# Kernel optimization log

Measured on AMD Instinct MI355X. Metric: run time of the kernel, lower is better.

The kernel has to match this reference:

```python
import jax, jax.numpy as jnp
import numpy as np

DIM = 1024
H = 16
HD = DIM // H  # 64
BASE = 10000.0


def _rope_tables(seq_len, d):
    # freqs over half-dim, then TILED (repeat) along last axis as in the torch code
    freqs = 1.0 / (BASE ** (jnp.arange(0, d, 2, dtype=jnp.float32) / d))  # [d/2]
    t = jnp.arange(seq_len, dtype=jnp.float32)
    f = jnp.outer(t, freqs)  # [S, d/2]
    cos = jnp.concatenate([jnp.cos(f), jnp.cos(f)], axis=-1)  # [S, d] (tiled, NOT interleaved)
    sin = jnp.concatenate([jnp.sin(f), jnp.sin(f)], axis=-1)
    return cos, sin


def _apply_rope(x):
    # x: [B, H, S, d]; rotation pairs adjacent elements (2i, 2i+1)
    S, d = x.shape[-2], x.shape[-1]
    cos, sin = _rope_tables(S, d)  # [S, d]
    xh = x.reshape(*x.shape[:-1], d // 2, 2)
    x_rot = jnp.stack([-xh[..., 1], xh[..., 0]], axis=-1).reshape(x.shape)
    return x * cos + x_rot * sin


def setup_inputs() -> dict:
    key = jax.random.key(0)
    ks = jax.random.split(key, 7)
    B, Sq, Sk = 16, 512, 512
    s = 0.02
    return {
        "x": jax.random.normal(ks[0], (B, Sq, DIM), jnp.float32),
        "context": jax.random.normal(ks[1], (B, Sk, DIM), jnp.float32),
        "Wq": jax.random.normal(ks[2], (DIM, DIM), jnp.float32) * s,
        "Wk": jax.random.normal(ks[3], (DIM, DIM), jnp.float32) * s,
        "Wv": jax.random.normal(ks[4], (DIM, DIM), jnp.float32) * s,
        "Wo": jax.random.normal(ks[5], (DIM, DIM), jnp.float32) * s,
        "bo": jax.random.normal(ks[6], (DIM,), jnp.float32) * s,
    }


def reference(x, context, Wq, Wk, Wv, Wo, bo):
    B, Sq, _ = x.shape
    Sk = context.shape[1]
    scale = HD ** -0.5
    # projections, split heads: [B, H, S, HD]
    q = (x @ Wq).reshape(B, Sq, H, HD).transpose(0, 2, 1, 3)
    k = (context @ Wk).reshape(B, Sk, H, HD).transpose(0, 2, 1, 3)
    v = (context @ Wv).reshape(B, Sk, H, HD).transpose(0, 2, 1, 3)
    q = _apply_rope(q)
    k = _apply_rope(k)
    attn = jax.nn.softmax(jnp.einsum("bhqd,bhkd->bhqk", q, k) * scale, axis=-1)
    out = jnp.einsum("bhqk,bhkd->bhqd", attn, v)
    out = out.transpose(0, 2, 1, 3).reshape(B, Sq, DIM)
    return out @ Wo + bo  # dropout is identity (p=0 / eval)
```

## Files before the change

kernel.cpp:

```cpp
#include <hip/hip_runtime.h>

#define DIM   1024
#define NH    16
#define HD    64
#define BATCH 16
#define SEQ   512
#define MROWS (BATCH*SEQ)
#define SL2E  0.18033688011112042f

typedef __bf16 bf16x8 __attribute__((ext_vector_type(8)));
typedef float  floatx4 __attribute__((ext_vector_type(4)));

static __device__ __forceinline__ unsigned short f2bf(float f) {
    union { float f; unsigned u; } v; v.f = f;
    unsigned u = v.u;
    return (unsigned short)((u + 0x7fffu + ((u >> 16) & 1u)) >> 16);
}

static __device__ __forceinline__ void glds16(const void* g, void* l) {
    __builtin_amdgcn_global_load_lds(
        (const __attribute__((address_space(1))) unsigned int*)g,
        (__attribute__((address_space(3))) unsigned int*)l, 16, 0, 0);
}

__global__ __launch_bounds__(256)
void rope_tab(float* __restrict__ ct, float* __restrict__ st)
{
    int id = blockIdx.x * blockDim.x + threadIdx.x;
    int d = id & (HD - 1), s = id >> 6;
    const float C = -0.41524101186092f;
    float f = exp2f((float)(d & 31) * C);
    float a = (float)s * f;
    ct[id] = cosf(a);
    st[id] = sinf(a);
}

__global__ __launch_bounds__(256)
void cvt_bf16(const float* __restrict__ X, const float* __restrict__ Cx,
              unsigned short* __restrict__ Xb, unsigned short* __restrict__ Cb)
{
    int id = blockIdx.x * blockDim.x + threadIdx.x;
    const float* src; unsigned short* dst; int e;
    if (id < (MROWS * DIM / 8)) { src = X;  dst = Xb; e = id * 8; }
    else                        { src = Cx; dst = Cb; e = (id - MROWS * DIM / 8) * 8; }
    float4 f0 = *(const float4*)&src[e];
    float4 f1 = *(const float4*)&src[e + 4];
    unsigned short o[8] = { f2bf(f0.x), f2bf(f0.y), f2bf(f0.z), f2bf(f0.w),
                            f2bf(f1.x), f2bf(f1.y), f2bf(f1.z), f2bf(f1.w) };
    *(uint4*)&dst[e] = *(const uint4*)o;
}

__global__ void transpose_w(const float* __restrict__ W0, const float* __restrict__ W1,
                            const float* __restrict__ W2, const float* __restrict__ W3,
                            unsigned short* __restrict__ T0, unsigned short* __restrict__ T1,
                            unsigned short* __restrict__ T2, unsigned short* __restrict__ T3)
{
    __shared__ float tile[32][33];
    const float* W; unsigned short* T;
    switch (blockIdx.z) {
        case 0:  W = W0; T = T0; break;
        case 1:  W = W1; T = T1; break;
        case 2:  W = W2; T = T2; break;
        default: W = W3; T = T3; break;
    }
    int n0 = blockIdx.x * 32, k0 = blockIdx.y * 32;
    int tx = threadIdx.x, ty = threadIdx.y;
    tile[ty][tx] = W[(size_t)(k0 + ty) * DIM + n0 + tx];
    __syncthreads();
    T[(size_t)(n0 + ty) * DIM + k0 + tx] = f2bf(tile[tx][ty]);
}

template <int MODE>
__global__ __launch_bounds__(256)
void gemm128(const unsigned short* __restrict__ A, const unsigned short* __restrict__ Bt,
             void* __restrict__ Out, const float* __restrict__ bias,
             const float* __restrict__ costab, const float* __restrict__ sintab)
{
    __shared__ unsigned short As[128 * 64];
    __shared__ unsigned short Bs[128 * 64];

    const int n0 = blockIdx.x * 128;
    const int m0 = blockIdx.y * 128;
    const int t  = threadIdx.x;
    const int w = t >> 6, l = t & 63;
    const int wm = w >> 1, wn = w & 1;
    const int lane16 = l & 15, quad = l >> 4;
    const int lr = l >> 3;
    const int lc = (l & 7) * 8;

    floatx4 acc[4][4];
    #pragma unroll
    for (int mi = 0; mi < 4; mi++)
        #pragma unroll
        for (int ni = 0; ni < 4; ni++) acc[mi][ni] = (floatx4){0.f, 0.f, 0.f, 0.f};

    for (int kt = 0; kt < DIM; kt += 64) {
        #pragma unroll
        for (int j = 0; j < 4; j++) {
            int ch = w * 4 + j;
            int row = ch * 8 + lr;
            glds16(A  + (size_t)(m0 + row) * DIM + kt + lc, &As[ch * 512]);
            glds16(Bt + (size_t)(n0 + row) * DIM + kt + lc, &Bs[ch * 512]);
        }
        __syncthreads();

        #pragma unroll
        for (int kk = 0; kk < 2; kk++) {
            bf16x8 af[4], bfr[4];
            #pragma unroll
            for (int mi = 0; mi < 4; mi++)
                af[mi] = *(const bf16x8*)&As[(wm * 64 + mi * 16 + lane16) * 64 + kk * 32 + quad * 8];
            #pragma unroll
            for (int ni = 0; ni < 4; ni++)
                bfr[ni] = *(const bf16x8*)&Bs[(wn * 64 + ni * 16 + lane16) * 64 + kk * 32 + quad * 8];
            #pragma unroll
            for (int mi = 0; mi < 4; mi++)
                #pragma unroll
                for (int ni = 0; ni < 4; ni++)
                    acc[mi][ni] = __builtin_amdgcn_mfma_f32_16x16x32_bf16(af[mi], bfr[ni], acc[mi][ni], 0, 0, 0);
        }
        __syncthreads();
    }

    if (MODE == 0) {
        unsigned short* O = (unsigned short*)Out;
        #pragma unroll
        for (int ni = 0; ni < 4; ni++) {
            int n = n0 + wn * 64 + ni * 16 + lane16;
            int h = n >> 6, d = n & 63;
            #pragma unroll
            for (int mi = 0; mi < 4; mi++) {
                #pragma unroll
                for (int i = 0; i < 4; i++) {
                    int m = m0 + wm * 64 + mi * 16 + quad * 4 + i;
                    int s = m & 511, b = m >> 9;
                    float v = acc[mi][ni][i];
                    float p = __shfl_xor(v, 1, 64);
                    float cs = costab[s * HD + d];
                    float sn = sintab[s * HD + d];
                    float r = (n & 1) ? fmaf(p, sn, v * cs) : fmaf(-p, sn, v * cs);
                    O[((size_t)(b * NH + h) * SEQ + s) * HD + d] = f2bf(r);
                }
            }
        }
    } else if (MODE == 1) {
        unsigned short* O = (unsigned short*)Out;
        #pragma unroll
        for (int mi = 0; mi < 4; mi++) {
            #pragma unroll
            for (int i = 0; i < 4; i++) {
                int m = m0 + wm * 64 + mi * 16 + quad * 4 + i;
                #pragma unroll
                for (int ni = 0; ni < 4; ni++) {
                    int n = n0 + wn * 64 + ni * 16 + lane16;
                    O[((size_t)(n >> 9) * DIM + m) * SEQ + (n & 511)] = f2bf(acc[mi][ni][i]);
                }
            }
        }
    } else {
        float* O = (float*)Out;
        #pragma unroll
        for (int ni = 0; ni < 4; ni++) {
            int n = n0 + wn * 64 + ni * 16 + lane16;
            float bv = bias[n];
            #pragma unroll
            for (int mi = 0; mi < 4; mi++) {
                #pragma unroll
                for (int i = 0; i < 4; i++) {
                    int m = m0 + wm * 64 + mi * 16 + quad * 4 + i;
                    O[(size_t)m * DIM + n] = acc[mi][ni][i] + bv;
                }
            }
        }
    }
}

__global__ __launch_bounds__(256)
void attn_v2(const unsigned short* __restrict__ Q, const unsigned short* __restrict__ K,
             const unsigned short* __restrict__ Vt, unsigned short* __restrict__ Out)
{
    __shared__ unsigned short Qs[64][72];
    __shared__ unsigned short Ks[64][72];
    __shared__ unsigned short Vts[64][72];
    __shared__ unsigned short Ps[64][72];

    const int id = blockIdx.x;
    const int qi = (id >> 3) & 7;
    const int bh = (id & 7) | ((id >> 6) << 3);
    const int q0 = qi * 64;
    const int t  = threadIdx.x;
    const int w = t >> 6, l = t & 63;
    const int lane16 = l & 15, quad = l >> 4;
    const size_t base = (size_t)bh * SEQ * HD;

    const int r = t >> 3, dd = (t & 7) * 8;
    *(uint4*)&Qs[r][dd]      = *(const uint4*)&Q[base + (size_t)(q0 + r) * HD + dd];
    *(uint4*)&Qs[r + 32][dd] = *(const uint4*)&Q[base + (size_t)(q0 + r + 32) * HD + dd];

    floatx4 acc_o[4];
    float lsum[4];
    #pragma unroll
    for (int c = 0; c < 4; c++) acc_o[c] = (floatx4){0.f, 0.f, 0.f, 0.f};
    #pragma unroll
    for (int i = 0; i < 4; i++) lsum[i] = 0.f;

    for (int kt = 0; kt < SEQ; kt += 64) {
        *(uint4*)&Ks[r][dd]       = *(const uint4*)&K[base + (size_t)(kt + r) * HD + dd];
        *(uint4*)&Ks[r + 32][dd]  = *(const uint4*)&K[base + (size_t)(kt + r + 32) * HD + dd];
        *(uint4*)&Vts[r][dd]      = *(const uint4*)&Vt[base + (size_t)r * SEQ + kt + dd];
        *(uint4*)&Vts[r + 32][dd] = *(const uint4*)&Vt[base + (size_t)(r + 32) * SEQ + kt + dd];
        __syncthreads();

        floatx4 sacc[4];
        #pragma unroll
        for (int c = 0; c < 4; c++) sacc[c] = (floatx4){0.f, 0.f, 0.f, 0.f};
        #pragma unroll
        for (int kk = 0; kk < 2; kk++) {
            bf16x8 a = *(const bf16x8*)&Qs[w * 16 + lane16][kk * 32 + quad * 8];
            #pragma unroll
            for (int c = 0; c < 4; c++) {
                bf16x8 b = *(const bf16x8*)&Ks[c * 16 + lane16][kk * 32 + quad * 8];
                sacc[c] = __builtin_amdgcn_mfma_f32_16x16x32_bf16(a, b, sacc[c], 0, 0, 0);
            }
        }

        #pragma unroll
        for (int i = 0; i < 4; i++) {
            #pragma unroll
            for (int c = 0; c < 4; c++) {
                float pv = exp2f(sacc[c][i] * SL2E);
                lsum[i] += pv;
                Ps[w * 16 + quad * 4 + i][c * 16 + lane16] = f2bf(pv);
            }
        }

        #pragma unroll
        for (int kk = 0; kk < 2; kk++) {
            bf16x8 a = *(const bf16x8*)&Ps[w * 16 + lane16][kk * 32 + quad * 8];
            #pragma unroll
            for (int c = 0; c < 4; c++) {
                bf16x8 b = *(const bf16x8*)&Vts[c * 16 + lane16][kk * 32 + quad * 8];
                acc_o[c] = __builtin_amdgcn_mfma_f32_16x16x32_bf16(a, b, acc_o[c], 0, 0, 0);
            }
        }
        __syncthreads();
    }

    const int b = bh >> 4, h = bh & 15;
    #pragma unroll
    for (int i = 0; i < 4; i++) {
        float rs = lsum[i];
        rs += __shfl_xor(rs, 1, 64);
        rs += __shfl_xor(rs, 2, 64);
        rs += __shfl_xor(rs, 4, 64);
        rs += __shfl_xor(rs, 8, 64);
        float inv = 1.0f / rs;
        int s = q0 + w * 16 + quad * 4 + i;
        #pragma unroll
        for (int c = 0; c < 4; c++) {
            int d = c * 16 + lane16;
            Out[((size_t)(b * SEQ + s)) * DIM + h * HD + d] = f2bf(acc_o[c][i] * inv);
        }
    }
}

extern "C" void kernel_launch(void* const* d_in, const int* in_sizes, int n_in,
                              void* d_out, int out_size, void* d_ws, size_t ws_size,
                              hipStream_t stream)
{
    const float* x   = (const float*)d_in[0];
    const float* ctx = (const float*)d_in[1];
    const float* Wq  = (const float*)d_in[2];
    const float* Wk  = (const float*)d_in[3];
    const float* Wv  = (const float*)d_in[4];
    const float* Wo  = (const float*)d_in[5];
    const float* bo  = (const float*)d_in[6];

    const size_t NW = (size_t)DIM * DIM;
    const size_t NB = (size_t)MROWS * DIM;

    unsigned short* x_bf   = (unsigned short*)d_ws;
    unsigned short* ctx_bf = x_bf + NB;
    unsigned short* WqT    = ctx_bf + NB;
    unsigned short* WkT    = WqT + NW;
    unsigned short* WvT    = WkT + NW;
    unsigned short* WoT    = WvT + NW;
    unsigned short* Kb     = WoT + NW;
    unsigned short* Vtb    = Kb + NB;
    float*          costab = (float*)(Vtb + NB);
    float*          sintab = costab + SEQ * HD;
    unsigned short* Qb     = ctx_bf;
    unsigned short* Ab     = x_bf;

    rope_tab<<<SEQ * HD / 256, 256, 0, stream>>>(costab, sintab);
    cvt_bf16<<<2 * MROWS * DIM / 8 / 256, 256, 0, stream>>>(x, ctx, x_bf, ctx_bf);
    transpose_w<<<dim3(32, 32, 4), dim3(32, 32, 1), 0, stream>>>(
        Wq, Wk, Wv, Wo, WqT, WkT, WvT, WoT);

    gemm128<0><<<dim3(DIM / 128, MROWS / 128), 256, 0, stream>>>(ctx_bf, WkT, Kb, nullptr, costab, sintab);
    gemm128<1><<<dim3(MROWS / 128, DIM / 128), 256, 0, stream>>>(WvT, ctx_bf, Vtb, nullptr, nullptr, nullptr);
    gemm128<0><<<dim3(DIM / 128, MROWS / 128), 256, 0, stream>>>(x_bf, WqT, Qb, nullptr, costab, sintab);

    attn_v2<<<2048, 256, 0, stream>>>(Qb, Kb, Vtb, Ab);

    gemm128<2><<<dim3(DIM / 128, MROWS / 128), 256, 0, stream>>>(Ab, WoT, d_out, bo, nullptr, nullptr);
}
```

Baseline: 292.4 us.

## Keep softmax probabilities in registers and double query tile per attention block

The attention kernel now computes S transposed (K as the A operand), so each lane's exp'd scores already sit in the layout the 16x16x16 bf16 MFMA expects for P. P is fed straight from registers to the PV product, which drops the Ps shared-memory round trip. Each block also handles 128 query rows instead of 64, halving the grid so every K/V tile load is reused twice, at the cost of more registers and a larger Q tile in LDS. The RoPE cos/sin tables are interleaved into a single float2 table so each GEMM epilogue element does one load instead of two.

```diff
diff --git a/kernel.cpp b/kernel.cpp
--- a/kernel.cpp
+++ b/kernel.cpp
@@ -10,6 +10,7 @@
 
 typedef __bf16 bf16x8 __attribute__((ext_vector_type(8)));
 typedef float  floatx4 __attribute__((ext_vector_type(4)));
+typedef short  short4v __attribute__((ext_vector_type(4)));
 
 static __device__ __forceinline__ unsigned short f2bf(float f) {
     union { float f; unsigned u; } v; v.f = f;
@@ -24,15 +25,14 @@
 }
 
 __global__ __launch_bounds__(256)
-void rope_tab(float* __restrict__ ct, float* __restrict__ st)
+void rope_tab(float2* __restrict__ cs)
 {
     int id = blockIdx.x * blockDim.x + threadIdx.x;
     int d = id & (HD - 1), s = id >> 6;
     const float C = -0.41524101186092f;
     float f = exp2f((float)(d & 31) * C);
     float a = (float)s * f;
-    ct[id] = cosf(a);
-    st[id] = sinf(a);
+    cs[id] = make_float2(cosf(a), sinf(a));
 }
 
 __global__ __launch_bounds__(256)
@@ -74,7 +74,7 @@
 __global__ __launch_bounds__(256)
 void gemm128(const unsigned short* __restrict__ A, const unsigned short* __restrict__ Bt,
              void* __restrict__ Out, const float* __restrict__ bias,
-             const float* __restrict__ costab, const float* __restrict__ sintab)
+             const float2* __restrict__ cstab)
 {
     __shared__ unsigned short As[128 * 64];
     __shared__ unsigned short Bs[128 * 64];
@@ -136,9 +136,8 @@
                     int s = m & 511, b = m >> 9;
                     float v = acc[mi][ni][i];
                     float p = __shfl_xor(v, 1, 64);
-                    float cs = costab[s * HD + d];
-                    float sn = sintab[s * HD + d];
-                    float r = (n & 1) ? fmaf(p, sn, v * cs) : fmaf(-p, sn, v * cs);
+                    float2 cs = cstab[s * HD + d];
+                    float r = (n & 1) ? fmaf(p, cs.y, v * cs.x) : fmaf(-p, cs.y, v * cs.x);
                     O[((size_t)(b * NH + h) * SEQ + s) * HD + d] = f2bf(r);
                 }
             }
@@ -175,91 +174,99 @@
     }
 }
 
-__global__ __launch_bounds__(256)
-void attn_v2(const unsigned short* __restrict__ Q, const unsigned short* __restrict__ K,
+__global__ __launch_bounds__(256, 4)
+void attn_v3(const unsigned short* __restrict__ Q, const unsigned short* __restrict__ K,
              const unsigned short* __restrict__ Vt, unsigned short* __restrict__ Out)
 {
-    __shared__ unsigned short Qs[64][72];
+    __shared__ unsigned short Qs[128][72];
     __shared__ unsigned short Ks[64][72];
     __shared__ unsigned short Vts[64][72];
-    __shared__ unsigned short Ps[64][72];
 
     const int id = blockIdx.x;
-    const int qi = (id >> 3) & 7;
-    const int bh = (id & 7) | ((id >> 6) << 3);
-    const int q0 = qi * 64;
+    const int qi = (id >> 3) & 3;
+    const int bh = (id & 7) | ((id >> 5) << 3);
+    const int q0 = qi * 128;
     const int t  = threadIdx.x;
     const int w = t >> 6, l = t & 63;
     const int lane16 = l & 15, quad = l >> 4;
     const size_t base = (size_t)bh * SEQ * HD;
 
-    const int r = t >> 3, dd = (t & 7) * 8;
-    *(uint4*)&Qs[r][dd]      = *(const uint4*)&Q[base + (size_t)(q0 + r) * HD + dd];
-    *(uint4*)&Qs[r + 32][dd] = *(const uint4*)&Q[base + (size_t)(q0 + r + 32) * HD + dd];
-
-    floatx4 acc_o[4];
-    float lsum[4];
+    const int sr = t >> 3, sc = (t & 7) * 8;
     #pragma unroll
-    for (int c = 0; c < 4; c++) acc_o[c] = (floatx4){0.f, 0.f, 0.f, 0.f};
+    for (int j = 0; j < 4; j++)
+        *(uint4*)&Qs[j * 32 + sr][sc] =
+            *(const uint4*)&Q[base + (size_t)(q0 + j * 32 + sr) * HD + sc];
+
+    floatx4 acc_o[2][4];
+    float lsum[2] = {0.f, 0.f};
     #pragma unroll
-    for (int i = 0; i < 4; i++) lsum[i] = 0.f;
+    for (int st = 0; st < 2; st++)
+        #pragma unroll
+        for (int dt = 0; dt < 4; dt++) acc_o[st][dt] = (floatx4){0.f, 0.f, 0.f, 0.f};
 
     for (int kt = 0; kt < SEQ; kt += 64) {
-        *(uint4*)&Ks[r][dd]       = *(const uint4*)&K[base + (size_t)(kt + r) * HD + dd];
-        *(uint4*)&Ks[r + 32][dd]  = *(const uint4*)&K[base + (size_t)(kt + r + 32) * HD + dd];
-        *(uint4*)&Vts[r][dd]      = *(const uint4*)&Vt[base + (size_t)r * SEQ + kt + dd];
-        *(uint4*)&Vts[r + 32][dd] = *(const uint4*)&Vt[base + (size_t)(r + 32) * SEQ + kt + dd];
         __syncthreads();
-
-        floatx4 sacc[4];
-        #pragma unroll
-        for (int c = 0; c < 4; c++) sacc[c] = (floatx4){0.f, 0.f, 0.f, 0.f};
-        #pragma unroll
-        for (int kk = 0; kk < 2; kk++) {
-            bf16x8 a = *(const bf16x8*)&Qs[w * 16 + lane16][kk * 32 + quad * 8];
+        *(uint4*)&Ks[sr][sc]       = *(const uint4*)&K[base + (size_t)(kt + sr) * HD + sc];
+        *(uint4*)&Ks[sr + 32][sc]  = *(const uint4*)&K[base + (size_t)(kt + sr + 32) * HD + sc];
+        *(uint4*)&Vts[sr][sc]      = *(const uint4*)&Vt[base + (size_t)sr * SEQ + kt + sc];
+        *(uint4*)&Vts[sr + 32][sc] = *(const uint4*)&Vt[base + (size_t)(sr + 32) * SEQ + kt + sc];
+        __syncthreads();
+
+        short4v pa[2][4];
+        #pragma unroll
+        for (int st = 0; st < 2; st++) {
+            floatx4 sacc[4];
+            #pragma unroll
+            for (int c = 0; c < 4; c++) sacc[c] = (floatx4){0.f, 0.f, 0.f, 0.f};
+            #pragma unroll
+            for (int kk = 0; kk < 2; kk++) {
+                bf16x8 qf = *(const bf16x8*)&Qs[st * 64 + w * 16 + lane16][kk * 32 + quad * 8];
+                #pragma unroll
+                for (int c = 0; c < 4; c++) {
+                    bf16x8 kf = *(const bf16x8*)&Ks[c * 16 + lane16][kk * 32 + quad * 8];
+                    sacc[c] = __builtin_amdgcn_mfma_f32_16x16x32_bf16(kf, qf, sacc[c], 0, 0, 0);
+                }
+            }
             #pragma unroll
             for (int c = 0; c < 4; c++) {
-                bf16x8 b = *(const bf16x8*)&Ks[c * 16 + lane16][kk * 32 + quad * 8];
-                sacc[c] = __builtin_amdgcn_mfma_f32_16x16x32_bf16(a, b, sacc[c], 0, 0, 0);
-            }
-        }
-
-        #pragma unroll
-        for (int i = 0; i < 4; i++) {
-            #pragma unroll
-            for (int c = 0; c < 4; c++) {
-                float pv = exp2f(sacc[c][i] * SL2E);
-                lsum[i] += pv;
-                Ps[w * 16 + quad * 4 + i][c * 16 + lane16] = f2bf(pv);
-            }
-        }
-
-        #pragma unroll
-        for (int kk = 0; kk < 2; kk++) {
-            bf16x8 a = *(const bf16x8*)&Ps[w * 16 + lane16][kk * 32 + quad * 8];
-            #pragma unroll
-            for (int c = 0; c < 4; c++) {
-                bf16x8 b = *(const bf16x8*)&Vts[c * 16 + lane16][kk * 32 + quad * 8];
-                acc_o[c] = __builtin_amdgcn_mfma_f32_16x16x32_bf16(a, b, acc_o[c], 0, 0, 0);
-            }
-        }
-        __syncthreads();
+                short4v pk;
+                #pragma unroll
+                for (int i = 0; i < 4; i++) {
+                    float pv = exp2f(sacc[c][i] * SL2E);
+                    lsum[st] += pv;
+                    pk[i] = (short)f2bf(pv);
+                }
+                pa[st][c] = pk;
+            }
+        }
+        #pragma unroll
+        for (int c = 0; c < 4; c++) {
+            #pragma unroll
+            for (int dt = 0; dt < 4; dt++) {
+                short4v vf = *(const short4v*)&Vts[dt * 16 + lane16][c * 16 + quad * 4];
+                #pragma unroll
+                for (int st = 0; st < 2; st++)
+                    acc_o[st][dt] = __builtin_amdgcn_mfma_f32_16x16x16bf16_1k(
+                        pa[st][c], vf, acc_o[st][dt], 0, 0, 0);
+            }
+        }
     }
 
     const int b = bh >> 4, h = bh & 15;
     #pragma unroll
-    for (int i = 0; i < 4; i++) {
-        float rs = lsum[i];
-        rs += __shfl_xor(rs, 1, 64);
-        rs += __shfl_xor(rs, 2, 64);
-        rs += __shfl_xor(rs, 4, 64);
-        rs += __shfl_xor(rs, 8, 64);
-        float inv = 1.0f / rs;
-        int s = q0 + w * 16 + quad * 4 + i;
-        #pragma unroll
-        for (int c = 0; c < 4; c++) {
-            int d = c * 16 + lane16;
-            Out[((size_t)(b * SEQ + s)) * DIM + h * HD + d] = f2bf(acc_o[c][i] * inv);
+    for (int st = 0; st < 2; st++) {
+        float rs = lsum[st];
+        rs += __shfl_xor(rs, 16, 64);
+        rs += __shfl_xor(rs, 32, 64);
+        #pragma unroll
+        for (int i = 0; i < 4; i++) {
+            float inv = 1.0f / __shfl(rs, quad * 4 + i, 64);
+            int s = q0 + st * 64 + w * 16 + quad * 4 + i;
+            #pragma unroll
+            for (int dt = 0; dt < 4; dt++) {
+                int d = dt * 16 + lane16;
+                Out[((size_t)(b * SEQ + s)) * DIM + h * HD + d] = f2bf(acc_o[st][dt][i] * inv);
+            }
         }
     }
 }
@@ -287,21 +294,20 @@
     unsigned short* WoT    = WvT + NW;
     unsigned short* Kb     = WoT + NW;
     unsigned short* Vtb    = Kb + NB;
-    float*          costab = (float*)(Vtb + NB);
-    float*          sintab = costab + SEQ * HD;
+    float2*         cstab  = (float2*)(Vtb + NB);
     unsigned short* Qb     = ctx_bf;
     unsigned short* Ab     = x_bf;
 
-    rope_tab<<<SEQ * HD / 256, 256, 0, stream>>>(costab, sintab);
+    rope_tab<<<SEQ * HD / 256, 256, 0, stream>>>(cstab);
     cvt_bf16<<<2 * MROWS * DIM / 8 / 256, 256, 0, stream>>>(x, ctx, x_bf, ctx_bf);
     transpose_w<<<dim3(32, 32, 4), dim3(32, 32, 1), 0, stream>>>(
         Wq, Wk, Wv, Wo, WqT, WkT, WvT, WoT);
 
-    gemm128<0><<<dim3(DIM / 128, MROWS / 128), 256, 0, stream>>>(ctx_bf, WkT, Kb, nullptr, costab, sintab);
-    gemm128<1><<<dim3(MROWS / 128, DIM / 128), 256, 0, stream>>>(WvT, ctx_bf, Vtb, nullptr, nullptr, nullptr);
-    gemm128<0><<<dim3(DIM / 128, MROWS / 128), 256, 0, stream>>>(x_bf, WqT, Qb, nullptr, costab, sintab);
-
-    attn_v2<<<2048, 256, 0, stream>>>(Qb, Kb, Vtb, Ab);
-
-    gemm128<2><<<dim3(DIM / 128, MROWS / 128), 256, 0, stream>>>(Ab, WoT, d_out, bo, nullptr, nullptr);
-}
+    gemm128<0><<<dim3(DIM / 128, MROWS / 128), 256, 0, stream>>>(ctx_bf, WkT, Kb, nullptr, cstab);
+    gemm128<1><<<dim3(MROWS / 128, DIM / 128), 256, 0, stream>>>(WvT, ctx_bf, Vtb, nullptr, nullptr);
+    gemm128<0><<<dim3(DIM / 128, MROWS / 128), 256, 0, stream>>>(x_bf, WqT, Qb, nullptr, cstab);
+
+    attn_v3<<<1024, 256, 0, stream>>>(Qb, Kb, Vtb, Ab);
+
+    gemm128<2><<<dim3(DIM / 128, MROWS / 128), 256, 0, stream>>>(Ab, WoT, d_out, bo, nullptr);
+}
```

Result: no change. 292.2 us (-0.1%).
